# Kernel optimization log

Hardware: AMD Instinct MI355X
Metric: run time of the kernel (lower is better)

## Reference

```python
import jax, jax.numpy as jnp
import numpy as np

N_NODES = 50000
N_EDGES = 600000
D_IN = 128
HIDDEN = 128
N_REL = 8
N_LAYERS = 2


def setup_inputs() -> dict:
    key = jax.random.key(0)
    ks = jax.random.split(key, 10)
    node_feat = jax.random.normal(ks[0], (N_NODES, D_IN), dtype=jnp.float32)
    edge_index = jax.random.randint(ks[1], (2, N_EDGES), 0, N_NODES, dtype=jnp.int64)
    edge_type = jax.random.randint(ks[2], (N_EDGES,), 0, N_REL, dtype=jnp.int64)
    s = 1.0 / np.sqrt(D_IN)
    # stacked per-layer FastRGCNConv params (input_dim == hidden so shapes match)
    rel_w = jax.random.normal(ks[3], (N_LAYERS, N_REL, D_IN, HIDDEN), dtype=jnp.float32) * s
    root_w = jax.random.normal(ks[4], (N_LAYERS, D_IN, HIDDEN), dtype=jnp.float32) * s
    bias = jax.random.normal(ks[5], (N_LAYERS, HIDDEN), dtype=jnp.float32) * 0.01
    proj_w = jax.random.normal(ks[6], (N_LAYERS * HIDDEN, HIDDEN), dtype=jnp.float32) / np.sqrt(N_LAYERS * HIDDEN)
    proj_b = jax.random.normal(ks[7], (HIDDEN,), dtype=jnp.float32) * 0.01
    return {
        "node_feat": node_feat,
        "edge_index": edge_index,
        "edge_type": edge_type,
        "rel_w": rel_w,
        "root_w": root_w,
        "bias": bias,
        "proj_w": proj_w,
        "proj_b": proj_b,
    }


def _rgcn_layer(x, src, dst, etype, W, root, b):
    # FastRGCNConv: transform all nodes by all relations, then gather per edge.
    xW = jnp.einsum('nd,rdh->nrh', x, W)          # [N, R, H]
    m = xW[src, etype]                             # [E, H] per-edge message
    # mean aggregation per (target, relation), as in PyG FastRGCNConv aggr='mean'
    seg = dst * N_REL + etype                      # combined (target, relation) id
    cnt = jax.ops.segment_sum(jnp.ones_like(etype, dtype=x.dtype), seg,
                              num_segments=N_NODES * N_REL)
    norm = (1.0 / jnp.clip(cnt, 1.0, None))[seg]   # [E]
    agg = jax.ops.segment_sum(m * norm[:, None], dst, num_segments=N_NODES)
    return agg + x @ root + b


def reference(node_feat, edge_index, edge_type, rel_w, root_w, bias, proj_w, proj_b):
    src, dst = edge_index[0], edge_index[1]
    reps = []
    h = node_feat
    for i in range(N_LAYERS):
        h = _rgcn_layer(h, src, dst, edge_type, rel_w[i], root_w[i], bias[i])
        h = jax.nn.relu(h)
        reps.append(h)
    final = jnp.concatenate(reps, axis=-1) @ proj_w + proj_b
    return (final,) + tuple(reps)
```

## Files before the change

kernel.cpp:

```cpp
#include <hip/hip_runtime.h>
#include <hip/hip_bf16.h>

#define NN 50000
#define NE 600000
#define DD 128
#define RR 8
#define KY 1152

#define N2 (NN * RR)
#define SCHUNK 1024
#define NBS2 ((N2 + SCHUNK - 1) / SCHUNK)
#define MGRID ((NN + 127) / 128)

typedef __attribute__((ext_vector_type(8))) short short8;
typedef __attribute__((ext_vector_type(4))) float f32x4;
typedef __attribute__((ext_vector_type(4))) unsigned uint4v;

__device__ __forceinline__ unsigned short f2b(float x){
  __hip_bfloat16 h = __float2bfloat16(x);
  return __builtin_bit_cast(unsigned short, h);
}
__device__ __forceinline__ float blo(unsigned u){ return __builtin_bit_cast(float, u << 16); }
__device__ __forceinline__ float bhi(unsigned u){ return __builtin_bit_cast(float, u & 0xFFFF0000u); }
__device__ __forceinline__ unsigned pack2(float a, float b){
  return (unsigned)f2b(a) | ((unsigned)f2b(b) << 16);
}

#define GLDS16(g, l) __builtin_amdgcn_global_load_lds( \
    (const __attribute__((address_space(1))) void*)(g), \
    (__attribute__((address_space(3))) void*)(l), 16, 0, 0)

__global__ __launch_bounds__(256) void k_hist(const int* __restrict__ ei,
                                              const int* __restrict__ et,
                                              int* __restrict__ cnt) {
  int e = blockIdx.x * 256 + threadIdx.x;
  if (e < NE) {
    int dst = ei[NE + e];
    int r = et[e];
    atomicAdd(&cnt[dst * RR + r], 1);
  }
}

__global__ __launch_bounds__(256) void k_scan1(const int* __restrict__ cnt,
                                               int* __restrict__ bsum) {
  int b = blockIdx.x, t = threadIdx.x;
  int base = b * SCHUNK + t * 4;
  int s = 0;
  if (base < N2) {
    int4 v = *(const int4*)&cnt[base];
    s = v.x + v.y + v.z + v.w;
  }
  #pragma unroll
  for (int off = 32; off; off >>= 1) s += __shfl_down(s, off);
  __shared__ int wsum[4];
  int lane = t & 63, wv = t >> 6;
  if (lane == 0) wsum[wv] = s;
  __syncthreads();
  if (t == 0) bsum[b] = wsum[0] + wsum[1] + wsum[2] + wsum[3];
}

__global__ __launch_bounds__(512) void k_scan2(const int* __restrict__ bsum,
                                               int* __restrict__ boff) {
  int t = threadIdx.x, lane = t & 63, wv = t >> 6;
  int v = (t < NBS2) ? bsum[t] : 0;
  int x = v;
  #pragma unroll
  for (int off = 1; off < 64; off <<= 1) {
    int y = __shfl_up(x, off);
    if (lane >= off) x += y;
  }
  __shared__ int wt[8];
  if (lane == 63) wt[wv] = x;
  __syncthreads();
  int woff = 0;
  for (int w = 0; w < wv; w++) woff += wt[w];
  if (t < NBS2) boff[t] = woff + x - v;
}

__global__ __launch_bounds__(256) void k_scan3(const int* __restrict__ cnt,
                                               const int* __restrict__ boff,
                                               int* __restrict__ rp2,
                                               int* __restrict__ cur2) {
  int b = blockIdx.x, t = threadIdx.x;
  int lane = t & 63, wv = t >> 6;
  int base = b * SCHUNK + t * 4;
  int v[4] = {0, 0, 0, 0};
  int s = 0;
  if (base < N2) {
    int4 q = *(const int4*)&cnt[base];
    v[0] = q.x; v[1] = q.y; v[2] = q.z; v[3] = q.w;
    s = q.x + q.y + q.z + q.w;
  }
  int x = s;
  #pragma unroll
  for (int off = 1; off < 64; off <<= 1) {
    int y = __shfl_up(x, off);
    if (lane >= off) x += y;
  }
  __shared__ int wtot[4];
  if (lane == 63) wtot[wv] = x;
  __syncthreads();
  int woff = 0;
  for (int w = 0; w < wv; w++) woff += wtot[w];
  int exc = boff[b] + woff + x - s;
  if (base < N2) {
    #pragma unroll
    for (int j = 0; j < 4; j++) {
      cur2[base + j] = exc;
      rp2[base + j + 1] = exc + v[j];
      exc += v[j];
    }
  }
  if (b == 0 && t == 0) rp2[0] = 0;
}

__global__ __launch_bounds__(256) void k_scatter(const int* __restrict__ ei,
                                                 const int* __restrict__ et,
                                                 int* __restrict__ cur2,
                                                 unsigned* __restrict__ packed) {
  int e = blockIdx.x * 256 + threadIdx.x;
  if (e < NE) {
    int src = ei[e];
    int dst = ei[NE + e];
    int r = et[e];
    int p = atomicAdd(&cur2[dst * RR + r], 1);
    packed[p] = (unsigned)src | ((unsigned)r << 16);
  }
}

__global__ __launch_bounds__(256) void k_xb(const float* __restrict__ x,
                                            unsigned* __restrict__ xb2) {
  int i = blockIdx.x * 256 + threadIdx.x;
  if (i < NN * (DD / 2)) {
    float2 v = ((const float2*)x)[i];
    xb2[i] = pack2(v.x, v.y);
  }
}

__global__ __launch_bounds__(256) void k_wt2(const float* __restrict__ rel_w,
                                             const float* __restrict__ root_w,
                                             unsigned short* __restrict__ WT2) {
  int idx = blockIdx.x * 256 + threadIdx.x;
  if (idx >= 2 * KY * DD) return;
  int k = idx % DD;
  int j = (idx / DD) % KY;
  int l = idx / (DD * KY);
  float v;
  if (j < RR * DD) v = rel_w[(((size_t)l * RR + (j >> 7)) * DD + k) * DD + (j & 127)];
  else             v = root_w[((size_t)l * DD + k) * DD + (j - RR * DD)];
  WT2[idx] = f2b(v);
}

__global__ __launch_bounds__(256) void k_pt(const float* __restrict__ proj_w,
                                            unsigned short* __restrict__ PT) {
  int idx = blockIdx.x * 256 + threadIdx.x;
  if (idx >= DD * 256) return;
  int k = idx % 256;
  int n = idx / 256;
  PT[idx] = f2b(proj_w[(size_t)k * DD + n]);
}

__global__ __launch_bounds__(512) void k_ygemm(const unsigned short* __restrict__ A, int lda,
                                               const unsigned short* __restrict__ B2,
                                               unsigned short* __restrict__ Y) {
  __shared__ unsigned short smA[128 * 128];
  int t = threadIdx.x;
  const int nb = MGRID * 9, q8 = nb >> 3, r8 = nb & 7;
  int xcd = blockIdx.x & 7, idx = blockIdx.x >> 3;
  int w = (xcd < r8 ? xcd * (q8 + 1) : r8 * (q8 + 1) + (xcd - r8) * q8) + idx;
  int rt = w / 9, ct = w % 9;

  int lane = t & 63, wv = t >> 6;
  int wm = wv >> 2, wn = wv & 3;
  int l15 = lane & 15, lk = lane >> 4;

  #pragma unroll
  for (int i = 0; i < 4; i++) {
    int f = i * 512 + t;
    int row = f >> 4, cl = f & 15;
    int cg = cl ^ (row & 15);
    int rg = rt * 128 + row; if (rg >= NN) rg = NN - 1;
    GLDS16(A + (size_t)rg * lda + cg * 8, &smA[f * 8]);
  }
  __syncthreads();

  short8 bf[4][2];
  #pragma unroll
  for (int kk = 0; kk < 4; kk++)
    #pragma unroll
    for (int q = 0; q < 2; q++) {
      int rb = ct * 128 + wn * 32 + q * 16 + l15;
      bf[kk][q] = *(const short8*)(B2 + (size_t)rb * DD + (kk * 4 + lk) * 8);
    }

  f32x4 acc[4][2];
  #pragma unroll
  for (int mi = 0; mi < 4; mi++)
    #pragma unroll
    for (int ni = 0; ni < 2; ni++)
      acc[mi][ni] = (f32x4){0.f, 0.f, 0.f, 0.f};

  #pragma unroll
  for (int kk = 0; kk < 4; kk++) {
    short8 af[4];
    int c = kk * 4 + lk;
    #pragma unroll
    for (int q = 0; q < 4; q++) {
      int r = wm * 64 + q * 16 + l15;
      af[q] = *(const short8*)&smA[r * 128 + ((c ^ (r & 15)) << 3)];
    }
    #pragma unroll
    for (int mi = 0; mi < 4; mi++)
      #pragma unroll
      for (int ni = 0; ni < 2; ni++)
        acc[mi][ni] = __builtin_amdgcn_mfma_f32_16x16x32_bf16(af[mi], bf[kk][ni], acc[mi][ni], 0, 0, 0);
  }

  #pragma unroll
  for (int mi = 0; mi < 4; mi++) {
    #pragma unroll
    for (int ni = 0; ni < 2; ni++) {
      int col = ct * 128 + wn * 32 + ni * 16 + l15;
      #pragma unroll
      for (int j = 0; j < 4; j++) {
        int rg = rt * 128 + wm * 64 + mi * 16 + lk * 4 + j;
        if (rg < NN) Y[(size_t)rg * KY + col] = f2b(acc[mi][ni][j]);
      }
    }
  }
}

__global__ __launch_bounds__(256) void k_aggD(const unsigned short* __restrict__ Y,
                                              const unsigned* __restrict__ packed,
                                              const int* __restrict__ rp2,
                                              const float* __restrict__ bias,
                                              float* __restrict__ outf,
                                              unsigned short* __restrict__ hb, int hboff) {
  int v = blockIdx.x * 4 + (threadIdx.x >> 6);
  int lane = threadIdx.x & 63;
  int q = lane >> 4, sub = lane & 15;

  int f = 0;
  if (lane <= 8) f = rp2[v * RR + lane];
  int fn = __shfl(f, lane + 1);
  int c = fn - f;
  float winv = (lane < 8 && c > 0) ? 1.f / (float)c : 0.f;
  int e0 = __shfl(f, 0), e1 = __shfl(f, 8);

  float acc[8];
  #pragma unroll
  for (int j = 0; j < 8; j++) acc[j] = 0.f;

  int e = e0 + q;
  unsigned rec = (e < e1) ? packed[e] : 0u;
  while (e < e1) {
    int en = e + 4;
    unsigned rec_next = (en < e1) ? packed[en] : 0u;
    int src = rec & 0xFFFF;
    int r = rec >> 16;
    float w = __shfl(winv, r);
    uint4v u = *(const uint4v*)(Y + (size_t)src * KY + r * DD + sub * 8);
    #pragma unroll
    for (int i = 0; i < 4; i++) {
      acc[2 * i]     += w * blo(u[i]);
      acc[2 * i + 1] += w * bhi(u[i]);
    }
    e = en; rec = rec_next;
  }

  if (q == 0) {
    uint4v u = *(const uint4v*)(Y + (size_t)v * KY + RR * DD + sub * 8);
    #pragma unroll
    for (int i = 0; i < 4; i++) {
      acc[2 * i]     += blo(u[i]);
      acc[2 * i + 1] += bhi(u[i]);
    }
  }

  #pragma unroll
  for (int j = 0; j < 8; j++) {
    acc[j] += __shfl_xor(acc[j], 32);
    acc[j] += __shfl_xor(acc[j], 16);
  }

  if (q == 0) {
    float4 b0 = *(const float4*)&bias[sub * 8];
    float4 b1 = *(const float4*)&bias[sub * 8 + 4];
    float val[8];
    val[0] = fmaxf(acc[0] + b0.x, 0.f); val[1] = fmaxf(acc[1] + b0.y, 0.f);
    val[2] = fmaxf(acc[2] + b0.z, 0.f); val[3] = fmaxf(acc[3] + b0.w, 0.f);
    val[4] = fmaxf(acc[4] + b1.x, 0.f); val[5] = fmaxf(acc[5] + b1.y, 0.f);
    val[6] = fmaxf(acc[6] + b1.z, 0.f); val[7] = fmaxf(acc[7] + b1.w, 0.f);
    float4* of = (float4*)&outf[(size_t)v * DD + sub * 8];
    of[0] = (float4){val[0], val[1], val[2], val[3]};
    of[1] = (float4){val[4], val[5], val[6], val[7]};
    uint4v hv;
    #pragma unroll
    for (int i = 0; i < 4; i++) hv[i] = pack2(val[2 * i], val[2 * i + 1]);
    *(uint4v*)(hb + (size_t)v * 256 + hboff + sub * 8) = hv;
  }
}

__global__ __launch_bounds__(256) void k_gemm(const unsigned short* __restrict__ A, int lda,
                                              const unsigned short* __restrict__ BT, int ldb,
                                              int M, int K,
                                              const float* __restrict__ bias,
                                              float* __restrict__ outf) {
  __shared__ unsigned short sA[128 * 64];
  __shared__ unsigned short sB[128 * 64];
  int t = threadIdx.x;
  int bm = blockIdx.x;
  int lane = t & 63, wv = t >> 6;
  int wm = wv >> 1, wn = wv & 1;
  int l15 = lane & 15, lk = lane >> 4;

  f32x4 acc[4][4];
  #pragma unroll
  for (int mi = 0; mi < 4; mi++)
    #pragma unroll
    for (int ni = 0; ni < 4; ni++)
      acc[mi][ni] = (f32x4){0.f, 0.f, 0.f, 0.f};

  int nkt = K >> 6;
  for (int kt = 0; kt < nkt; kt++) {
    #pragma unroll
    for (int i = 0; i < 4; i++) {
      int f = i * 256 + t;
      int row = f >> 3, cl = f & 7;
      int cg = cl ^ (row & 7);
      int rg = bm * 128 + row;
      if (rg >= M) rg = M - 1;
      GLDS16(A + (size_t)rg * lda + kt * 64 + cg * 8, &sA[f * 8]);
    }
    #pragma unroll
    for (int i = 0; i < 4; i++) {
      int f = i * 256 + t;
      int row = f >> 3, cl = f & 7;
      int cg = cl ^ (row & 7);
      GLDS16(BT + (size_t)row * ldb + kt * 64 + cg * 8, &sB[f * 8]);
    }
    __syncthreads();

    short8 af[4][2], bf[4][2];
    #pragma unroll
    for (int mi = 0; mi < 4; mi++) {
      #pragma unroll
      for (int kk = 0; kk < 2; kk++) {
        int r = wm * 64 + mi * 16 + l15;
        int c = kk * 4 + lk;
        af[mi][kk] = *(const short8*)&sA[((r << 3) + (c ^ (r & 7))) << 3];
        int rb = wn * 64 + mi * 16 + l15;
        bf[mi][kk] = *(const short8*)&sB[((rb << 3) + (c ^ (rb & 7))) << 3];
      }
    }
    #pragma unroll
    for (int mi = 0; mi < 4; mi++)
      #pragma unroll
      for (int ni = 0; ni < 4; ni++)
        #pragma unroll
        for (int kk = 0; kk < 2; kk++)
          acc[mi][ni] = __builtin_amdgcn_mfma_f32_16x16x32_bf16(af[mi][kk], bf[ni][kk], acc[mi][ni], 0, 0, 0);
    __syncthreads();
  }

  #pragma unroll
  for (int mi = 0; mi < 4; mi++) {
    #pragma unroll
    for (int ni = 0; ni < 4; ni++) {
      int cg = wn * 64 + ni * 16 + l15;
      float bv = bias[cg];
      #pragma unroll
      for (int j = 0; j < 4; j++) {
        int rg = bm * 128 + wm * 64 + mi * 16 + lk * 4 + j;
        if (rg < M) outf[(size_t)rg * 128 + cg] = acc[mi][ni][j] + bv;
      }
    }
  }
}

extern "C" void kernel_launch(void* const* d_in, const int* in_sizes, int n_in,
                              void* d_out, int out_size, void* d_ws, size_t ws_size,
                              hipStream_t stream) {
  const float* node_feat = (const float*)d_in[0];
  const int*   ei        = (const int*)d_in[1];
  const int*   et        = (const int*)d_in[2];
  const float* rel_w     = (const float*)d_in[3];
  const float* root_w    = (const float*)d_in[4];
  const float* bias      = (const float*)d_in[5];
  const float* proj_w    = (const float*)d_in[6];
  const float* proj_b    = (const float*)d_in[7];
  float* out = (float*)d_out;

  char* ws = (char*)d_ws;
  size_t off = 0;
  auto carve = [&](size_t bytes) { void* p = ws + off; off = (off + bytes + 255) & ~(size_t)255; return p; };
  unsigned short* Y    = (unsigned short*)carve((size_t)NN * KY * 2);
  unsigned short* Hb   = (unsigned short*)carve((size_t)NN * 256 * 2);
  unsigned short* xb   = (unsigned short*)carve((size_t)NN * DD * 2);
  unsigned short* WT2  = (unsigned short*)carve((size_t)2 * KY * DD * 2);
  unsigned short* PT   = (unsigned short*)carve((size_t)DD * 256 * 2);
  int* cnt_vr          = (int*)carve((size_t)N2 * 4);
  int* rp2             = (int*)carve((size_t)(N2 + 1) * 4);
  int* cur2            = (int*)carve((size_t)N2 * 4);
  unsigned* packed     = (unsigned*)carve((size_t)NE * 4);
  int* bsum            = (int*)carve((size_t)512 * 4);
  int* boff            = (int*)carve((size_t)512 * 4);
  (void)ws_size; (void)in_sizes; (void)n_in; (void)out_size;

  hipMemsetAsync(cnt_vr, 0, (size_t)N2 * 4, stream);

  int egrid = (NE + 255) / 256;
  k_hist<<<egrid, 256, 0, stream>>>(ei, et, cnt_vr);
  k_scan1<<<NBS2, 256, 0, stream>>>(cnt_vr, bsum);
  k_scan2<<<1, 512, 0, stream>>>(bsum, boff);
  k_scan3<<<NBS2, 256, 0, stream>>>(cnt_vr, boff, rp2, cur2);
  k_scatter<<<egrid, 256, 0, stream>>>(ei, et, cur2, packed);

  k_xb<<<(NN * (DD / 2) + 255) / 256, 256, 0, stream>>>(node_feat, (unsigned*)xb);
  k_wt2<<<(2 * KY * DD + 255) / 256, 256, 0, stream>>>(rel_w, root_w, WT2);
  k_pt<<<(DD * 256 + 255) / 256, 256, 0, stream>>>(proj_w, PT);

  k_ygemm<<<MGRID * 9, 512, 0, stream>>>(xb, DD, WT2, Y);
  k_aggD<<<NN / 4, 256, 0, stream>>>(Y, packed, rp2, bias,
                                     out + (size_t)NN * DD, Hb, 0);
  k_ygemm<<<MGRID * 9, 512, 0, stream>>>(Hb, 256, WT2 + (size_t)KY * DD, Y);
  k_aggD<<<NN / 4, 256, 0, stream>>>(Y, packed, rp2, bias + DD,
                                     out + (size_t)2 * NN * DD, Hb, DD);
  k_gemm<<<MGRID, 256, 0, stream>>>(Hb, 256, PT, 256, NN, 256, proj_b, out);
}
```

Baseline: 261.9 us.

## Reuse staged A tile across three column tiles with double-buffered B fragments

Each ygemm block now computes three 128-wide output column tiles instead of one, reusing the 128x128 A tile already staged in LDS, so the grid shrinks threefold. B fragments for the next column tile are prefetched into alternate registers while the current tile's MFMAs run. This cuts redundant global loads of A and per-block launch overhead, at the cost of more registers and fewer blocks to spread across CUs.

```diff
diff --git a/kernel.cpp b/kernel.cpp
--- a/kernel.cpp
+++ b/kernel.cpp
@@ -11,6 +11,7 @@
 #define SCHUNK 1024
 #define NBS2 ((N2 + SCHUNK - 1) / SCHUNK)
 #define MGRID ((NN + 127) / 128)
+#define NCT 3
 
 typedef __attribute__((ext_vector_type(8))) short short8;
 typedef __attribute__((ext_vector_type(4))) float f32x4;
@@ -165,10 +166,10 @@
                                                unsigned short* __restrict__ Y) {
   __shared__ unsigned short smA[128 * 128];
   int t = threadIdx.x;
-  const int nb = MGRID * 9, q8 = nb >> 3, r8 = nb & 7;
+  const int nb = MGRID * NCT, q8 = nb >> 3, r8 = nb & 7;
   int xcd = blockIdx.x & 7, idx = blockIdx.x >> 3;
   int w = (xcd < r8 ? xcd * (q8 + 1) : r8 * (q8 + 1) + (xcd - r8) * q8) + idx;
-  int rt = w / 9, ct = w % 9;
+  int rt = w / NCT, c3 = w % NCT;
 
   int lane = t & 63, wv = t >> 6;
   int wm = wv >> 2, wn = wv & 3;
@@ -184,47 +185,84 @@
   }
   __syncthreads();
 
-  short8 bf[4][2];
-  #pragma unroll
-  for (int kk = 0; kk < 4; kk++)
-    #pragma unroll
-    for (int q = 0; q < 2; q++) {
-      int rb = ct * 128 + wn * 32 + q * 16 + l15;
-      bf[kk][q] = *(const short8*)(B2 + (size_t)rb * DD + (kk * 4 + lk) * 8);
-    }
-
-  f32x4 acc[4][2];
-  #pragma unroll
-  for (int mi = 0; mi < 4; mi++)
-    #pragma unroll
-    for (int ni = 0; ni < 2; ni++)
-      acc[mi][ni] = (f32x4){0.f, 0.f, 0.f, 0.f};
-
-  #pragma unroll
-  for (int kk = 0; kk < 4; kk++) {
-    short8 af[4];
-    int c = kk * 4 + lk;
-    #pragma unroll
-    for (int q = 0; q < 4; q++) {
-      int r = wm * 64 + q * 16 + l15;
-      af[q] = *(const short8*)&smA[r * 128 + ((c ^ (r & 15)) << 3)];
-    }
+  short8 bfA[4][2], bfB[4][2];
+  {
+    int ct = c3 * NCT + 0;
+    #pragma unroll
+    for (int kk = 0; kk < 4; kk++)
+      #pragma unroll
+      for (int q = 0; q < 2; q++) {
+        int rb = ct * 128 + wn * 32 + q * 16 + l15;
+        bfA[kk][q] = *(const short8*)(B2 + (size_t)rb * DD + (kk * 4 + lk) * 8);
+      }
+  }
+
+  #pragma unroll
+  for (int i = 0; i < NCT; i++) {
+    int ct = c3 * NCT + i;
+
+    f32x4 acc[4][2];
     #pragma unroll
     for (int mi = 0; mi < 4; mi++)
       #pragma unroll
       for (int ni = 0; ni < 2; ni++)
-        acc[mi][ni] = __builtin_amdgcn_mfma_f32_16x16x32_bf16(af[mi], bf[kk][ni], acc[mi][ni], 0, 0, 0);
-  }
-
-  #pragma unroll
-  for (int mi = 0; mi < 4; mi++) {
-    #pragma unroll
-    for (int ni = 0; ni < 2; ni++) {
-      int col = ct * 128 + wn * 32 + ni * 16 + l15;
-      #pragma unroll
-      for (int j = 0; j < 4; j++) {
-        int rg = rt * 128 + wm * 64 + mi * 16 + lk * 4 + j;
-        if (rg < NN) Y[(size_t)rg * KY + col] = f2b(acc[mi][ni][j]);
+        acc[mi][ni] = (f32x4){0.f, 0.f, 0.f, 0.f};
+
+    #pragma unroll
+    for (int kk = 0; kk < 4; kk++) {
+      short8 af[4];
+      int c = kk * 4 + lk;
+      #pragma unroll
+      for (int q = 0; q < 4; q++) {
+        int r = wm * 64 + q * 16 + l15;
+        af[q] = *(const short8*)&smA[r * 128 + ((c ^ (r & 15)) << 3)];
+      }
+      if ((i & 1) == 0) {
+        #pragma unroll
+        for (int mi = 0; mi < 4; mi++)
+          #pragma unroll
+          for (int ni = 0; ni < 2; ni++)
+            acc[mi][ni] = __builtin_amdgcn_mfma_f32_16x16x32_bf16(af[mi], bfA[kk][ni], acc[mi][ni], 0, 0, 0);
+      } else {
+        #pragma unroll
+        for (int mi = 0; mi < 4; mi++)
+          #pragma unroll
+          for (int ni = 0; ni < 2; ni++)
+            acc[mi][ni] = __builtin_amdgcn_mfma_f32_16x16x32_bf16(af[mi], bfB[kk][ni], acc[mi][ni], 0, 0, 0);
+      }
+    }
+
+    if (i + 1 < NCT) {
+      int ctn = ct + 1;
+      if ((i & 1) == 0) {
+        #pragma unroll
+        for (int kk = 0; kk < 4; kk++)
+          #pragma unroll
+          for (int q = 0; q < 2; q++) {
+            int rb = ctn * 128 + wn * 32 + q * 16 + l15;
+            bfB[kk][q] = *(const short8*)(B2 + (size_t)rb * DD + (kk * 4 + lk) * 8);
+          }
+      } else {
+        #pragma unroll
+        for (int kk = 0; kk < 4; kk++)
+          #pragma unroll
+          for (int q = 0; q < 2; q++) {
+            int rb = ctn * 128 + wn * 32 + q * 16 + l15;
+            bfA[kk][q] = *(const short8*)(B2 + (size_t)rb * DD + (kk * 4 + lk) * 8);
+          }
+      }
+    }
+
+    #pragma unroll
+    for (int mi = 0; mi < 4; mi++) {
+      #pragma unroll
+      for (int ni = 0; ni < 2; ni++) {
+        int col = ct * 128 + wn * 32 + ni * 16 + l15;
+        #pragma unroll
+        for (int j = 0; j < 4; j++) {
+          int rg = rt * 128 + wm * 64 + mi * 16 + lk * 4 + j;
+          if (rg < NN) Y[(size_t)rg * KY + col] = f2b(acc[mi][ni][j]);
+        }
       }
     }
   }
@@ -420,10 +458,10 @@
   k_wt2<<<(2 * KY * DD + 255) / 256, 256, 0, stream>>>(rel_w, root_w, WT2);
   k_pt<<<(DD * 256 + 255) / 256, 256, 0, stream>>>(proj_w, PT);
 
-  k_ygemm<<<MGRID * 9, 512, 0, stream>>>(xb, DD, WT2, Y);
+  k_ygemm<<<MGRID * NCT, 512, 0, stream>>>(xb, DD, WT2, Y);
   k_aggD<<<NN / 4, 256, 0, stream>>>(Y, packed, rp2, bias,
                                      out + (size_t)NN * DD, Hb, 0);
-  k_ygemm<<<MGRID * 9, 512, 0, stream>>>(Hb, 256, WT2 + (size_t)KY * DD, Y);
+  k_ygemm<<<MGRID * NCT, 512, 0, stream>>>(Hb, 256, WT2 + (size_t)KY * DD, Y);
   k_aggD<<<NN / 4, 256, 0, stream>>>(Y, packed, rp2, bias + DD,
                                      out + (size_t)2 * NN * DD, Hb, DD);
   k_gemm<<<MGRID, 256, 0, stream>>>(Hb, 256, PT, 256, NN, 256, proj_b, out);
```

Result: slower. 271.0 us (+3.5%).
